# Kernel optimization log

Measured on AMD Instinct MI355X. Metric: run time of the kernel, lower is better.

The kernel has to match this reference:

```python
import jax, jax.numpy as jnp
import numpy as np

BN_EPS = 1e-5


def setup_inputs() -> dict:
    key = jax.random.key(0)
    ks = jax.random.split(key, 6)
    N, C, T, V, S = 64, 64, 300, 25, 3
    x = jax.random.normal(ks[0], (N, C, T, V), dtype=jnp.float32)
    A = jax.random.uniform(ks[1], (S, V, V), dtype=jnp.float32)
    PA1 = jnp.ones((S, V, V), dtype=jnp.float32)
    PA2 = jax.random.normal(ks[2], (S, V, V), dtype=jnp.float32) * 1e-3
    Wc = jax.random.normal(ks[3], (S, C, C), dtype=jnp.float32) * np.sqrt(2.0 / (C * S))
    bc = jnp.zeros((S, C), dtype=jnp.float32)
    gamma = jnp.ones((C,), dtype=jnp.float32)
    beta = jnp.zeros((C,), dtype=jnp.float32)
    rmean = jnp.zeros((C,), dtype=jnp.float32)
    rvar = jnp.ones((C,), dtype=jnp.float32)
    return {"x": x, "A": A, "PA1": PA1, "PA2": PA2, "Wc": Wc, "bc": bc,
            "gamma": gamma, "beta": beta, "rmean": rmean, "rvar": rvar}


def reference(x, A, PA1, PA2, Wc, bc, gamma, beta, rmean, rvar):
    # x: (N, C, T, V); A/PA1/PA2: (S, V, V); Wc: (S, out_c, in_c); bc: (S, out_c)
    Ae = A * PA1 + PA2  # adaptive adjacency, (S, V, V)
    S = Ae.shape[0]
    y = None
    for i in range(S):  # small fixed loop over graph subsets
        # graph aggregation over joints: (N,C,T,V) @ (V,V) -> (N,C,T,V)
        xa = jnp.einsum('nctv,vw->nctw', x, Ae[i])
        # 1x1 conv over channels + bias
        z = jnp.einsum('nctw,oc->notw', xa, Wc[i]) + bc[i][None, :, None, None]
        y = z if y is None else y + z
    # BatchNorm2d (inference form with running stats)
    scale = gamma / jnp.sqrt(rvar + BN_EPS)
    y = y * scale[None, :, None, None] + (beta - rmean * scale)[None, :, None, None]
    # residual: in_channels == out_channels -> down is identity
    y = y + x
    return jax.nn.relu(y)
```

## Files before the change

kernel.cpp:

```cpp
#include <hip/hip_runtime.h>

typedef _Float16 half_t;
typedef __attribute__((ext_vector_type(8))) _Float16 half8;
typedef __attribute__((ext_vector_type(4))) _Float16 half4;
typedef __attribute__((ext_vector_type(4))) float float4_t;

#define BN_EPS 1e-5f

constexpr int Nn = 64, Cc = 64, Tt = 300, Vv = 25, Ss = 3;
constexpr int TB   = 8;
constexpr int TWN  = TB * Vv;
constexpr int NT   = 13;
constexpr int XL_T = 32;
constexpr int XL_C = TB * XL_T + 8;
constexpr int XA_S = 72;
constexpr int XA_R = NT * 16;
constexpr int AE_S = 40;

__global__ __launch_bounds__(256, 2)
void gcn_fused(const float* __restrict__ x,   const float* __restrict__ A,
               const float* __restrict__ PA1, const float* __restrict__ PA2,
               const float* __restrict__ Wc,  const float* __restrict__ bc,
               const float* __restrict__ gamma, const float* __restrict__ beta,
               const float* __restrict__ rmean, const float* __restrict__ rvar,
               float* __restrict__ out)
{
    __shared__ __align__(16) half_t Xl[Cc * XL_C];
    __shared__ __align__(16) half_t xaL[XA_R * XA_S];
    __shared__ __align__(16) half_t AeT[Ss * 32 * AE_S];
    __shared__ float bnsc[Cc], bnsh[Cc];

    const int tid  = threadIdx.x;
    const int lane = tid & 63;
    const int wave = tid >> 6;
    const int col  = lane & 15;
    const int quad = lane >> 4;

    const int tb = blockIdx.x;
    const int n  = blockIdx.y;
    const int t0 = tb * TB;

    if (tid < Cc) {
        float sc   = gamma[tid] * rsqrtf(rvar[tid] + BN_EPS);
        float bsum = bc[tid] + bc[Cc + tid] + bc[2 * Cc + tid];
        bnsc[tid] = sc;
        bnsh[tid] = beta[tid] - rmean[tid] * sc + bsum * sc;
    }

    for (int e = tid; e < Ss * 32 * 32; e += 256) {
        int s = e >> 10, r = e & 1023, w = r >> 5, v = r & 31;
        float val = 0.f;
        if (v < Vv && w < Vv) {
            int ai = (s * Vv + v) * Vv + w;
            val = A[ai] * PA1[ai] + PA2[ai];
        }
        AeT[(s * 32 + w) * AE_S + v] = (half_t)val;
    }

    for (int e = tid; e < (XA_R - TWN) * XA_S; e += 256)
        xaL[TWN * XA_S + e] = (half_t)0.f;

    half8 wf[Ss][2];
    {
        int o = wave * 16 + col;
        #pragma unroll
        for (int s = 0; s < Ss; ++s)
            #pragma unroll
            for (int ks = 0; ks < 2; ++ks) {
                const float* p = Wc + (s * Cc + o) * Cc + ks * 32 + quad * 8;
                half8 h;
                #pragma unroll
                for (int j = 0; j < 8; ++j) h[j] = (half_t)p[j];
                wf[s][ks] = h;
            }
    }

    {
        const float* xb = x + (size_t)n * Cc * Tt * Vv + t0 * Vv;
        for (int slot = tid; slot < Cc * TB * 8; slot += 256) {
            int c = slot >> 6, rem = slot & 63, t = rem >> 3, k = rem & 7;
            int v0 = k * 4;
            half4 h;
            #pragma unroll
            for (int j = 0; j < 4; ++j) {
                int v = v0 + j;
                float f = (v < Vv && (t0 + t) < Tt) ? xb[c * Tt * Vv + t * Vv + v] : 0.f;
                h[j] = (half_t)f;
            }
            *(half4*)&Xl[c * XL_C + t * XL_T + v0] = h;
        }
    }
    __syncthreads();

    const float4_t zero4 = {0.f, 0.f, 0.f, 0.f};
    float4_t yacc[NT];
    #pragma unroll
    for (int i = 0; i < NT; ++i) yacc[i] = zero4;

    for (int s = 0; s < Ss; ++s) {
        half8 ab[2];
        #pragma unroll
        for (int wt = 0; wt < 2; ++wt)
            ab[wt] = *(const half8*)&AeT[(s * 32 + wt * 16 + col) * AE_S + quad * 8];

        #pragma unroll
        for (int ti = 0; ti < 2; ++ti) {
            int t = wave * 2 + ti;
            #pragma unroll
            for (int ct = 0; ct < 4; ++ct) {
                half8 af = *(const half8*)&Xl[(ct * 16 + col) * XL_C + t * XL_T + quad * 8];
                #pragma unroll
                for (int wt = 0; wt < 2; ++wt) {
                    float4_t r = __builtin_amdgcn_mfma_f32_16x16x32_f16(af, ab[wt], zero4, 0, 0, 0);
                    int w = wt * 16 + col;
                    if (w < Vv) {
                        half4 h;
                        #pragma unroll
                        for (int i = 0; i < 4; ++i) h[i] = (half_t)r[i];
                        *(half4*)&xaL[(t * Vv + w) * XA_S + ct * 16 + quad * 4] = h;
                    }
                }
            }
        }
        __syncthreads();

        #pragma unroll
        for (int nt = 0; nt < NT; ++nt) {
            int tw = nt * 16 + col;
            #pragma unroll
            for (int ks = 0; ks < 2; ++ks) {
                half8 bf = *(const half8*)&xaL[tw * XA_S + ks * 32 + quad * 8];
                yacc[nt] = __builtin_amdgcn_mfma_f32_16x16x32_f16(wf[s][ks], bf, yacc[nt], 0, 0, 0);
            }
        }
        __syncthreads();
    }

    const int limit = min(TWN, (Tt - t0) * Vv);
    float* ob = out + (size_t)n * Cc * Tt * Vv + t0 * Vv;
    #pragma unroll
    for (int nt = 0; nt < NT; ++nt) {
        int tw = nt * 16 + col;
        if (tw < limit) {
            int t = tw / Vv;
            int w = tw - t * Vv;
            #pragma unroll
            for (int i = 0; i < 4; ++i) {
                int o = wave * 16 + quad * 4 + i;
                float val = yacc[nt][i] * bnsc[o] + bnsh[o];
                val += (float)Xl[o * XL_C + t * XL_T + w];
                ob[o * Tt * Vv + tw] = fmaxf(val, 0.f);
            }
        }
    }
}

extern "C" void kernel_launch(void* const* d_in, const int* in_sizes, int n_in,
                              void* d_out, int out_size, void* d_ws, size_t ws_size,
                              hipStream_t stream) {
    const float* x     = (const float*)d_in[0];
    const float* A     = (const float*)d_in[1];
    const float* PA1   = (const float*)d_in[2];
    const float* PA2   = (const float*)d_in[3];
    const float* Wc    = (const float*)d_in[4];
    const float* bc    = (const float*)d_in[5];
    const float* gamma = (const float*)d_in[6];
    const float* beta  = (const float*)d_in[7];
    const float* rmean = (const float*)d_in[8];
    const float* rvar  = (const float*)d_in[9];
    float* out = (float*)d_out;

    dim3 grid((Tt + TB - 1) / TB, Nn);
    gcn_fused<<<grid, 256, 0, stream>>>(x, A, PA1, PA2, Wc, bc, gamma, beta, rmean, rvar, out);
}
```

Baseline: 351.8 us.

## Halve time tile, raise occupancy, vectorize loads, alias adjacency into scratch LDS

Shrinks the per-block time tile from 8 to 4 frames so each wave handles one frame, and raises the occupancy hint to 4 blocks per CU. The adjacency matrices are staged through the xa scratch buffer and kept in registers, which frees their LDS and drops one barrier. Global loads of x and Wc become float4 vector loads with padding zeroed separately, and the final sync and tail bounds checks are removed because 300 divides by 4. In exchange there are twice as many blocks, so per-block setup and Wc/adjacency reloads are repeated more often, and register pressure is tighter under the higher occupancy bound.

```diff
diff --git a/kernel.cpp b/kernel.cpp
--- a/kernel.cpp
+++ b/kernel.cpp
@@ -8,16 +8,16 @@
 #define BN_EPS 1e-5f
 
 constexpr int Nn = 64, Cc = 64, Tt = 300, Vv = 25, Ss = 3;
-constexpr int TB   = 8;
+constexpr int TB   = 4;
 constexpr int TWN  = TB * Vv;
-constexpr int NT   = 13;
+constexpr int NT   = 7;
 constexpr int XL_T = 32;
 constexpr int XL_C = TB * XL_T + 8;
 constexpr int XA_S = 72;
 constexpr int XA_R = NT * 16;
 constexpr int AE_S = 40;
 
-__global__ __launch_bounds__(256, 2)
+__global__ __launch_bounds__(256, 4)
 void gcn_fused(const float* __restrict__ x,   const float* __restrict__ A,
                const float* __restrict__ PA1, const float* __restrict__ PA2,
                const float* __restrict__ Wc,  const float* __restrict__ bc,
@@ -27,8 +27,9 @@
 {
     __shared__ __align__(16) half_t Xl[Cc * XL_C];
     __shared__ __align__(16) half_t xaL[XA_R * XA_S];
-    __shared__ __align__(16) half_t AeT[Ss * 32 * AE_S];
     __shared__ float bnsc[Cc], bnsh[Cc];
+
+    half_t* AeU = xaL;
 
     const int tid  = threadIdx.x;
     const int lane = tid & 63;
@@ -54,11 +55,16 @@
             int ai = (s * Vv + v) * Vv + w;
             val = A[ai] * PA1[ai] + PA2[ai];
         }
-        AeT[(s * 32 + w) * AE_S + v] = (half_t)val;
+        AeU[(s * 32 + w) * AE_S + v] = (half_t)val;
     }
 
     for (int e = tid; e < (XA_R - TWN) * XA_S; e += 256)
         xaL[TWN * XA_S + e] = (half_t)0.f;
+
+    for (int e = tid; e < Cc * TB * 7; e += 256) {
+        int c = e / 28, r = e % 28, t = r / 7, v = 25 + r % 7;
+        Xl[c * XL_C + t * XL_T + v] = (half_t)0.f;
+    }
 
     half8 wf[Ss][2];
     {
@@ -68,28 +74,37 @@
             #pragma unroll
             for (int ks = 0; ks < 2; ++ks) {
                 const float* p = Wc + (s * Cc + o) * Cc + ks * 32 + quad * 8;
+                float4_t a = *(const float4_t*)p;
+                float4_t b = *(const float4_t*)(p + 4);
                 half8 h;
                 #pragma unroll
-                for (int j = 0; j < 8; ++j) h[j] = (half_t)p[j];
+                for (int j = 0; j < 4; ++j) { h[j] = (half_t)a[j]; h[4 + j] = (half_t)b[j]; }
                 wf[s][ks] = h;
             }
     }
 
     {
         const float* xb = x + (size_t)n * Cc * Tt * Vv + t0 * Vv;
-        for (int slot = tid; slot < Cc * TB * 8; slot += 256) {
-            int c = slot >> 6, rem = slot & 63, t = rem >> 3, k = rem & 7;
-            int v0 = k * 4;
-            half4 h;
+        for (int i = tid; i < Cc * (TWN / 4); i += 256) {
+            int c = i / 25, k = i - c * 25;
+            float4_t f = *(const float4_t*)(xb + c * (Tt * Vv) + k * 4);
+            int p = k * 4;
             #pragma unroll
             for (int j = 0; j < 4; ++j) {
-                int v = v0 + j;
-                float f = (v < Vv && (t0 + t) < Tt) ? xb[c * Tt * Vv + t * Vv + v] : 0.f;
-                h[j] = (half_t)f;
+                int g = p + j;
+                int t = g / 25, v = g - t * 25;
+                Xl[c * XL_C + t * XL_T + v] = (half_t)f[j];
             }
-            *(half4*)&Xl[c * XL_C + t * XL_T + v0] = h;
         }
     }
+    __syncthreads();
+
+    half8 ab[Ss][2];
+    #pragma unroll
+    for (int s = 0; s < Ss; ++s)
+        #pragma unroll
+        for (int wt = 0; wt < 2; ++wt)
+            ab[s][wt] = *(const half8*)&AeU[(s * 32 + wt * 16 + col) * AE_S + quad * 8];
     __syncthreads();
 
     const float4_t zero4 = {0.f, 0.f, 0.f, 0.f};
@@ -97,28 +112,22 @@
     #pragma unroll
     for (int i = 0; i < NT; ++i) yacc[i] = zero4;
 
+    const int t = wave;
+
+    #pragma unroll
     for (int s = 0; s < Ss; ++s) {
-        half8 ab[2];
         #pragma unroll
-        for (int wt = 0; wt < 2; ++wt)
-            ab[wt] = *(const half8*)&AeT[(s * 32 + wt * 16 + col) * AE_S + quad * 8];
-
-        #pragma unroll
-        for (int ti = 0; ti < 2; ++ti) {
-            int t = wave * 2 + ti;
+        for (int ct = 0; ct < 4; ++ct) {
+            half8 af = *(const half8*)&Xl[(ct * 16 + col) * XL_C + t * XL_T + quad * 8];
             #pragma unroll
-            for (int ct = 0; ct < 4; ++ct) {
-                half8 af = *(const half8*)&Xl[(ct * 16 + col) * XL_C + t * XL_T + quad * 8];
-                #pragma unroll
-                for (int wt = 0; wt < 2; ++wt) {
-                    float4_t r = __builtin_amdgcn_mfma_f32_16x16x32_f16(af, ab[wt], zero4, 0, 0, 0);
-                    int w = wt * 16 + col;
-                    if (w < Vv) {
-                        half4 h;
-                        #pragma unroll
-                        for (int i = 0; i < 4; ++i) h[i] = (half_t)r[i];
-                        *(half4*)&xaL[(t * Vv + w) * XA_S + ct * 16 + quad * 4] = h;
-                    }
+            for (int wt = 0; wt < 2; ++wt) {
+                float4_t r = __builtin_amdgcn_mfma_f32_16x16x32_f16(af, ab[s][wt], zero4, 0, 0, 0);
+                int w = wt * 16 + col;
+                if (w < Vv) {
+                    half4 h;
+                    #pragma unroll
+                    for (int i2 = 0; i2 < 4; ++i2) h[i2] = (half_t)r[i2];
+                    *(half4*)&xaL[(t * Vv + w) * XA_S + ct * 16 + quad * 4] = h;
                 }
             }
         }
@@ -133,22 +142,21 @@
                 yacc[nt] = __builtin_amdgcn_mfma_f32_16x16x32_f16(wf[s][ks], bf, yacc[nt], 0, 0, 0);
             }
         }
-        __syncthreads();
+        if (s != Ss - 1) __syncthreads();
     }
 
-    const int limit = min(TWN, (Tt - t0) * Vv);
     float* ob = out + (size_t)n * Cc * Tt * Vv + t0 * Vv;
     #pragma unroll
     for (int nt = 0; nt < NT; ++nt) {
         int tw = nt * 16 + col;
-        if (tw < limit) {
-            int t = tw / Vv;
-            int w = tw - t * Vv;
+        if (tw < TWN) {
+            int tt = tw / 25;
+            int w  = tw - tt * 25;
             #pragma unroll
             for (int i = 0; i < 4; ++i) {
                 int o = wave * 16 + quad * 4 + i;
                 float val = yacc[nt][i] * bnsc[o] + bnsh[o];
-                val += (float)Xl[o * XL_C + t * XL_T + w];
+                val += (float)Xl[o * XL_C + tt * XL_T + w];
                 ob[o * Tt * Vv + tw] = fmaxf(val, 0.f);
             }
         }
@@ -170,6 +178,6 @@
     const float* rvar  = (const float*)d_in[9];
     float* out = (float*)d_out;
 
-    dim3 grid((Tt + TB - 1) / TB, Nn);
+    dim3 grid(Tt / TB, Nn);
     gcn_fused<<<grid, 256, 0, stream>>>(x, A, PA1, PA2, Wc, bc, gamma, beta, rmean, rvar, out);
 }
```

New measurement: 320.1 us. 1.1x faster.

## Split weight prep into pre-kernel and make main kernel wave-per-timestep without block syncs

Applied to the files above, without the earlier changes.

A tiny pre-kernel computes the adaptive adjacency, the fp16 MFMA-fragment-packed weights and the folded BN scale/shift into workspace. The main kernel assigns one timestep per wave and loads x straight from global into registers. Each wave uses its own double-buffered LDS slice for the intermediate, which removes block-wide __syncthreads and shrinks LDS so occupancy can rise to 4 blocks per CU. In exchange every wave re-reads the packed weights from global or cache, x is read twice (once for the MFMA input, once for the residual), and a second kernel launch is added.

```diff
diff --git a/kernel.cpp b/kernel.cpp
--- a/kernel.cpp
+++ b/kernel.cpp
@@ -4,31 +4,62 @@
 typedef __attribute__((ext_vector_type(8))) _Float16 half8;
 typedef __attribute__((ext_vector_type(4))) _Float16 half4;
 typedef __attribute__((ext_vector_type(4))) float float4_t;
+typedef float f4u __attribute__((ext_vector_type(4), aligned(4)));
 
 #define BN_EPS 1e-5f
 
 constexpr int Nn = 64, Cc = 64, Tt = 300, Vv = 25, Ss = 3;
-constexpr int TB   = 8;
-constexpr int TWN  = TB * Vv;
-constexpr int NT   = 13;
-constexpr int XL_T = 32;
-constexpr int XL_C = TB * XL_T + 8;
 constexpr int XA_S = 72;
-constexpr int XA_R = NT * 16;
-constexpr int AE_S = 40;
 
-__global__ __launch_bounds__(256, 2)
-void gcn_fused(const float* __restrict__ x,   const float* __restrict__ A,
-               const float* __restrict__ PA1, const float* __restrict__ PA2,
-               const float* __restrict__ Wc,  const float* __restrict__ bc,
-               const float* __restrict__ gamma, const float* __restrict__ beta,
-               const float* __restrict__ rmean, const float* __restrict__ rvar,
-               float* __restrict__ out)
+__global__ __launch_bounds__(256, 1)
+void gcn_pre(const float* __restrict__ A,   const float* __restrict__ PA1,
+             const float* __restrict__ PA2, const float* __restrict__ Wc,
+             const float* __restrict__ bc,  const float* __restrict__ gamma,
+             const float* __restrict__ beta, const float* __restrict__ rmean,
+             const float* __restrict__ rvar,
+             half_t* __restrict__ aeh, half_t* __restrict__ wch,
+             float* __restrict__ bnsc, float* __restrict__ bnsh)
 {
-    __shared__ __align__(16) half_t Xl[Cc * XL_C];
-    __shared__ __align__(16) half_t xaL[XA_R * XA_S];
-    __shared__ __align__(16) half_t AeT[Ss * 32 * AE_S];
-    __shared__ float bnsc[Cc], bnsh[Cc];
+    const int tid = threadIdx.x;
+    if (tid < Cc) {
+        float sc   = gamma[tid] * rsqrtf(rvar[tid] + BN_EPS);
+        float bsum = bc[tid] + bc[Cc + tid] + bc[2 * Cc + tid];
+        bnsc[tid] = sc;
+        bnsh[tid] = beta[tid] - rmean[tid] * sc + bsum * sc;
+    }
+    for (int e = tid; e < Ss * 2 * 64; e += 256) {
+        int s = e >> 7, wt = (e >> 6) & 1, lane = e & 63;
+        int col = lane & 15, q = lane >> 4;
+        int w = wt * 16 + col;
+        #pragma unroll
+        for (int j = 0; j < 8; ++j) {
+            int v = q * 8 + j;
+            float val = 0.f;
+            if (v < Vv && w < Vv) {
+                int ai = (s * Vv + v) * Vv + w;
+                val = A[ai] * PA1[ai] + PA2[ai];
+            }
+            aeh[e * 8 + j] = (half_t)val;
+        }
+    }
+    for (int e = tid; e < Ss * 4 * 2 * 64; e += 256) {
+        int s = e >> 9, r = e & 511, ot = r >> 7, ks = (r >> 6) & 1, lane = r & 63;
+        int col = lane & 15, q = lane >> 4;
+        int o = ot * 16 + col;
+        #pragma unroll
+        for (int j = 0; j < 8; ++j) {
+            int c = ks * 32 + q * 8 + j;
+            wch[e * 8 + j] = (half_t)Wc[(s * Cc + o) * Cc + c];
+        }
+    }
+}
+
+__global__ __launch_bounds__(256, 4)
+void gcn_main(const float* __restrict__ x, const half_t* __restrict__ aeh,
+              const half_t* __restrict__ wch, const float* __restrict__ bnsc,
+              const float* __restrict__ bnsh, float* __restrict__ out)
+{
+    __shared__ __align__(16) half_t xaW[4][2][32][XA_S];
 
     const int tid  = threadIdx.x;
     const int lane = tid & 63;
@@ -36,120 +67,89 @@
     const int col  = lane & 15;
     const int quad = lane >> 4;
 
-    const int tb = blockIdx.x;
     const int n  = blockIdx.y;
-    const int t0 = tb * TB;
+    const int tg = blockIdx.x * 4 + wave;
 
-    if (tid < Cc) {
-        float sc   = gamma[tid] * rsqrtf(rvar[tid] + BN_EPS);
-        float bsum = bc[tid] + bc[Cc + tid] + bc[2 * Cc + tid];
-        bnsc[tid] = sc;
-        bnsh[tid] = beta[tid] - rmean[tid] * sc + bsum * sc;
+    half8 ab[Ss][2];
+    #pragma unroll
+    for (int s = 0; s < Ss; ++s)
+        #pragma unroll
+        for (int wt = 0; wt < 2; ++wt)
+            ab[s][wt] = *(const half8*)&aeh[((s * 2 + wt) * 64 + lane) * 8];
+
+    half8 af[4];
+    #pragma unroll
+    for (int ct = 0; ct < 4; ++ct) {
+        const float* p = x + ((size_t)(n * Cc + ct * 16 + col) * Tt + tg) * Vv;
+        half8 h;
+        if (quad < 3) {
+            f4u a0 = *(const f4u*)(p + quad * 8);
+            f4u a1 = *(const f4u*)(p + quad * 8 + 4);
+            #pragma unroll
+            for (int j = 0; j < 4; ++j) { h[j] = (half_t)a0[j]; h[4 + j] = (half_t)a1[j]; }
+        } else {
+            h[0] = (half_t)p[24];
+            #pragma unroll
+            for (int j = 1; j < 8; ++j) h[j] = (half_t)0.f;
+        }
+        af[ct] = h;
     }
 
-    for (int e = tid; e < Ss * 32 * 32; e += 256) {
-        int s = e >> 10, r = e & 1023, w = r >> 5, v = r & 31;
-        float val = 0.f;
-        if (v < Vv && w < Vv) {
-            int ai = (s * Vv + v) * Vv + w;
-            val = A[ai] * PA1[ai] + PA2[ai];
+    const float4_t zero4 = {0.f, 0.f, 0.f, 0.f};
+    float4_t yacc[4][2];
+    #pragma unroll
+    for (int ot = 0; ot < 4; ++ot)
+        #pragma unroll
+        for (int wt = 0; wt < 2; ++wt) yacc[ot][wt] = zero4;
+
+    #pragma unroll
+    for (int s = 0; s < Ss; ++s) {
+        const int sb = s & 1;
+        #pragma unroll
+        for (int ct = 0; ct < 4; ++ct)
+            #pragma unroll
+            for (int wt = 0; wt < 2; ++wt) {
+                float4_t r = __builtin_amdgcn_mfma_f32_16x16x32_f16(af[ct], ab[s][wt], zero4, 0, 0, 0);
+                half4 h;
+                #pragma unroll
+                for (int i = 0; i < 4; ++i) h[i] = (half_t)r[i];
+                *(half4*)&xaW[wave][sb][wt * 16 + col][ct * 16 + quad * 4] = h;
+            }
+        half8 bf[2][2];
+        #pragma unroll
+        for (int ks = 0; ks < 2; ++ks)
+            #pragma unroll
+            for (int wt = 0; wt < 2; ++wt)
+                bf[ks][wt] = *(const half8*)&xaW[wave][sb][wt * 16 + col][ks * 32 + quad * 8];
+        #pragma unroll
+        for (int ot = 0; ot < 4; ++ot) {
+            half8 w0 = *(const half8*)&wch[(((s * 4 + ot) * 2 + 0) * 64 + lane) * 8];
+            half8 w1 = *(const half8*)&wch[(((s * 4 + ot) * 2 + 1) * 64 + lane) * 8];
+            #pragma unroll
+            for (int wt = 0; wt < 2; ++wt) {
+                yacc[ot][wt] = __builtin_amdgcn_mfma_f32_16x16x32_f16(w0, bf[0][wt], yacc[ot][wt], 0, 0, 0);
+                yacc[ot][wt] = __builtin_amdgcn_mfma_f32_16x16x32_f16(w1, bf[1][wt], yacc[ot][wt], 0, 0, 0);
+            }
         }
-        AeT[(s * 32 + w) * AE_S + v] = (half_t)val;
     }
 
-    for (int e = tid; e < (XA_R - TWN) * XA_S; e += 256)
-        xaL[TWN * XA_S + e] = (half_t)0.f;
-
-    half8 wf[Ss][2];
-    {
-        int o = wave * 16 + col;
+    const size_t base = (size_t)n * Cc * Tt * Vv + (size_t)tg * Vv;
+    const float* xr   = x + base;
+    float* outr       = out + base;
+    #pragma unroll
+    for (int ot = 0; ot < 4; ++ot) {
+        float4_t sc = *(const float4_t*)&bnsc[ot * 16 + quad * 4];
+        float4_t sh = *(const float4_t*)&bnsh[ot * 16 + quad * 4];
         #pragma unroll
-        for (int s = 0; s < Ss; ++s)
+        for (int i = 0; i < 4; ++i) {
+            const size_t ro = (size_t)(ot * 16 + quad * 4 + i) * (Tt * Vv);
             #pragma unroll
-            for (int ks = 0; ks < 2; ++ks) {
-                const float* p = Wc + (s * Cc + o) * Cc + ks * 32 + quad * 8;
-                half8 h;
-                #pragma unroll
-                for (int j = 0; j < 8; ++j) h[j] = (half_t)p[j];
-                wf[s][ks] = h;
-            }
-    }
-
-    {
-        const float* xb = x + (size_t)n * Cc * Tt * Vv + t0 * Vv;
-        for (int slot = tid; slot < Cc * TB * 8; slot += 256) {
-            int c = slot >> 6, rem = slot & 63, t = rem >> 3, k = rem & 7;
-            int v0 = k * 4;
-            half4 h;
-            #pragma unroll
-            for (int j = 0; j < 4; ++j) {
-                int v = v0 + j;
-                float f = (v < Vv && (t0 + t) < Tt) ? xb[c * Tt * Vv + t * Vv + v] : 0.f;
-                h[j] = (half_t)f;
-            }
-            *(half4*)&Xl[c * XL_C + t * XL_T + v0] = h;
-        }
-    }
-    __syncthreads();
-
-    const float4_t zero4 = {0.f, 0.f, 0.f, 0.f};
-    float4_t yacc[NT];
-    #pragma unroll
-    for (int i = 0; i < NT; ++i) yacc[i] = zero4;
-
-    for (int s = 0; s < Ss; ++s) {
-        half8 ab[2];
-        #pragma unroll
-        for (int wt = 0; wt < 2; ++wt)
-            ab[wt] = *(const half8*)&AeT[(s * 32 + wt * 16 + col) * AE_S + quad * 8];
-
-        #pragma unroll
-        for (int ti = 0; ti < 2; ++ti) {
-            int t = wave * 2 + ti;
-            #pragma unroll
-            for (int ct = 0; ct < 4; ++ct) {
-                half8 af = *(const half8*)&Xl[(ct * 16 + col) * XL_C + t * XL_T + quad * 8];
-                #pragma unroll
-                for (int wt = 0; wt < 2; ++wt) {
-                    float4_t r = __builtin_amdgcn_mfma_f32_16x16x32_f16(af, ab[wt], zero4, 0, 0, 0);
-                    int w = wt * 16 + col;
-                    if (w < Vv) {
-                        half4 h;
-                        #pragma unroll
-                        for (int i = 0; i < 4; ++i) h[i] = (half_t)r[i];
-                        *(half4*)&xaL[(t * Vv + w) * XA_S + ct * 16 + quad * 4] = h;
-                    }
+            for (int wt = 0; wt < 2; ++wt) {
+                int w = wt * 16 + col;
+                if (w < Vv) {
+                    float val = yacc[ot][wt][i] * sc[i] + sh[i] + xr[ro + w];
+                    outr[ro + w] = fmaxf(val, 0.f);
                 }
-            }
-        }
-        __syncthreads();
-
-        #pragma unroll
-        for (int nt = 0; nt < NT; ++nt) {
-            int tw = nt * 16 + col;
-            #pragma unroll
-            for (int ks = 0; ks < 2; ++ks) {
-                half8 bf = *(const half8*)&xaL[tw * XA_S + ks * 32 + quad * 8];
-                yacc[nt] = __builtin_amdgcn_mfma_f32_16x16x32_f16(wf[s][ks], bf, yacc[nt], 0, 0, 0);
-            }
-        }
-        __syncthreads();
-    }
-
-    const int limit = min(TWN, (Tt - t0) * Vv);
-    float* ob = out + (size_t)n * Cc * Tt * Vv + t0 * Vv;
-    #pragma unroll
-    for (int nt = 0; nt < NT; ++nt) {
-        int tw = nt * 16 + col;
-        if (tw < limit) {
-            int t = tw / Vv;
-            int w = tw - t * Vv;
-            #pragma unroll
-            for (int i = 0; i < 4; ++i) {
-                int o = wave * 16 + quad * 4 + i;
-                float val = yacc[nt][i] * bnsc[o] + bnsh[o];
-                val += (float)Xl[o * XL_C + t * XL_T + w];
-                ob[o * Tt * Vv + tw] = fmaxf(val, 0.f);
             }
         }
     }
@@ -170,6 +170,12 @@
     const float* rvar  = (const float*)d_in[9];
     float* out = (float*)d_out;
 
-    dim3 grid((Tt + TB - 1) / TB, Nn);
-    gcn_fused<<<grid, 256, 0, stream>>>(x, A, PA1, PA2, Wc, bc, gamma, beta, rmean, rvar, out);
+    half_t* aeh = (half_t*)d_ws;
+    half_t* wch = aeh + Ss * 2 * 64 * 8;
+    float* bnsc = (float*)(wch + Ss * 4 * 2 * 64 * 8);
+    float* bnsh = bnsc + Cc;
+
+    gcn_pre<<<dim3(1), 256, 0, stream>>>(A, PA1, PA2, Wc, bc, gamma, beta, rmean, rvar,
+                                         aeh, wch, bnsc, bnsh);
+    gcn_main<<<dim3(Tt / 4, Nn), 256, 0, stream>>>(x, aeh, wch, bnsc, bnsh, out);
 }
```

Result: faster. 319.4 us (-9.2%).
